# Kernel tuning notes

Measured on AMD Instinct MI355X. Metric: run time of the kernel, lower is better.

The kernel has to match this reference:

```python
import jax, jax.numpy as jnp
import numpy as np

N, C, HD, E, T, HS, WS = 8, 256, 8, 64, 16, 14, 14
S = HS * WS
EPS = 1e-5
FACTOR = 1.0 / np.sqrt(S * E).astype(np.float32)


def hswish(x):
    return x * jnp.clip(x + 3.0, 0.0, 6.0) * (1.0 / 6.0)


def _bn(x, g, b, m, v):
    shp = (1, -1, 1, 1, 1)
    scale = g / jnp.sqrt(v + EPS)
    return (x - m.reshape(shp)) * scale.reshape(shp) + b.reshape(shp)


def _dwconv(x, w):
    # depthwise Conv3d kernel (1,3,3), padding (0,1,1), groups=C
    return jax.lax.conv_general_dilated(
        x, w, window_strides=(1, 1, 1),
        padding=((0, 0), (1, 1), (1, 1)),
        dimension_numbers=('NCDHW', 'OIDHW', 'NCDHW'),
        feature_group_count=x.shape[1])


def _project(x, dw, g1, b1, m1, v1, pw, pb=None, bn2=None):
    h = hswish(_bn(_dwconv(x, dw), g1, b1, m1, v1))
    y = jnp.einsum('ncthw,oc->nothw', h, pw)
    if pb is not None:
        y = y + pb.reshape(1, -1, 1, 1, 1)
    if bn2 is not None:
        y = _bn(y, *bn2)
    return y


def setup_inputs() -> dict:
    key = jax.random.key(0)
    ks = jax.random.split(key, 8)
    d = {}
    d['x'] = jax.random.normal(ks[0], (N, C, T, HS, WS), jnp.float32)
    for name, k, out in (('theta', ks[1], HD * E), ('phi', ks[2], HD * E), ('g', ks[3], HD * C)):
        k1, k2 = jax.random.split(k)
        d[name + '_dw'] = jax.random.normal(k1, (C, 1, 1, 3, 3), jnp.float32) * 0.2
        d[name + '_bn1_g'] = jnp.ones((C,), jnp.float32)
        d[name + '_bn1_b'] = jnp.zeros((C,), jnp.float32)
        d[name + '_bn1_m'] = jnp.zeros((C,), jnp.float32)
        d[name + '_bn1_v'] = jnp.ones((C,), jnp.float32)
        d[name + '_pw'] = jax.random.normal(k2, (out, C), jnp.float32) * (1.0 / np.sqrt(C).astype(np.float32))
    d['theta_pb'] = jnp.zeros((HD * E,), jnp.float32)
    d['phi_pb'] = jnp.zeros((HD * E,), jnp.float32)
    d['g_bn2_g'] = jnp.ones((HD * C,), jnp.float32)
    d['g_bn2_b'] = jnp.zeros((HD * C,), jnp.float32)
    d['g_bn2_m'] = jnp.zeros((HD * C,), jnp.float32)
    d['g_bn2_v'] = jnp.ones((HD * C,), jnp.float32)
    d['heads_w'] = jax.random.normal(ks[4], (HD, HD), jnp.float32)
    return d


def reference(x, theta_dw, theta_bn1_g, theta_bn1_b, theta_bn1_m, theta_bn1_v, theta_pw, theta_pb,
              phi_dw, phi_bn1_g, phi_bn1_b, phi_bn1_m, phi_bn1_v, phi_pw, phi_pb,
              g_dw, g_bn1_g, g_bn1_b, g_bn1_m, g_bn1_v, g_pw,
              g_bn2_g, g_bn2_b, g_bn2_m, g_bn2_v, heads_w):
    th = _project(x, theta_dw, theta_bn1_g, theta_bn1_b, theta_bn1_m, theta_bn1_v, theta_pw, pb=theta_pb)
    ph = _project(x, phi_dw, phi_bn1_g, phi_bn1_b, phi_bn1_m, phi_bn1_v, phi_pw, pb=phi_pb)
    gg = hswish(_project(x, g_dw, g_bn1_g, g_bn1_b, g_bn1_m, g_bn1_v, g_pw,
                         bn2=(g_bn2_g, g_bn2_b, g_bn2_m, g_bn2_v)))
    TH = th.reshape(N, HD, E, T, S)   # theta features
    PH = ph.reshape(N, HD, E, T, S)   # phi features
    G5 = gg.reshape(N, HD, C, T, S)   # value features
    # adjacency over temporal nodes: [N,H,T,T]
    adj = jax.nn.softmax(FACTOR * jnp.einsum('nhets,nheus->nhtu', TH, PH), axis=-1)
    # GCN step: [N,H,T,C,S]
    gcn = hswish(jnp.einsum('nhtu,nhcus->nhtcs', adj, G5))
    # head-mix attention: [N,T,H]
    hf = gcn.mean(axis=(3, 4)).transpose(0, 2, 1)
    attn = jax.nn.softmax(hf @ heads_w, axis=-1)
    # combine heads: [N,C,T,S] -> [N,C,T,Hs,Ws]
    z = jnp.einsum('nhtcs,nth->ncts', gcn, attn).reshape(N, C, T, HS, WS)
    return hswish(x + z)
```

## Files before the change

### kernel.cpp

```cpp
#include <hip/hip_runtime.h>
#include <hip/hip_bf16.h>

typedef __hip_bfloat16 bf16;
typedef __attribute__((ext_vector_type(4))) float f32x4;
typedef __attribute__((ext_vector_type(8))) short s16x8;

#define DEV static __device__ __forceinline__

namespace {

constexpr float kEPS = 1e-5f;
constexpr float kFACTOR = 1.0f / 112.0f;

DEV float hswish_f(float v) { return v * fminf(fmaxf(v + 3.f, 0.f), 6.f) * (1.f / 6.f); }

__global__ void cvt_pw_kernel(const float* __restrict__ a,
                              const float* __restrict__ b,
                              const float* __restrict__ cG,
                              const float* __restrict__ g2g, const float* __restrict__ g2b,
                              const float* __restrict__ g2m, const float* __restrict__ g2v,
                              bf16* __restrict__ oa, bf16* __restrict__ ob,
                              bf16* __restrict__ oc, float* __restrict__ bnscl,
                              float* __restrict__ bnsft) {
  int i = blockIdx.x * 256 + threadIdx.x;
  if (i < 512 * 256) {
    oa[i] = __float2bfloat16(a[i]);
    ob[i] = __float2bfloat16(b[i]);
  }
  if (i < 2048 * 256) {
    int r = i >> 8, k = i & 255;
    int h = r >> 8, c = r & 255;
    oc[(c * 8 + h) * 256 + k] = __float2bfloat16(cG[i]);
  }
  if (i < 2048) {
    int c = i >> 3, h = i & 7, ref = h * 256 + c;
    float s = g2g[ref] * rsqrtf(g2v[ref] + kEPS);
    bnscl[i] = s;
    bnsft[i] = g2b[ref] - g2m[ref] * s;
  }
}

__global__ __launch_bounds__(256) void conv_kernel(
    const float* __restrict__ x,
    const float* __restrict__ tdw, const float* __restrict__ tg,
    const float* __restrict__ tb, const float* __restrict__ tm, const float* __restrict__ tv,
    const float* __restrict__ pdw, const float* __restrict__ pg,
    const float* __restrict__ pb, const float* __restrict__ pm, const float* __restrict__ pv,
    const float* __restrict__ gdw, const float* __restrict__ gG,
    const float* __restrict__ gb, const float* __restrict__ gm, const float* __restrict__ gv,
    bf16* __restrict__ h_t, bf16* __restrict__ h_p, bf16* __restrict__ h_g) {
  int bid = blockIdx.x;
  int cb = bid & 3, t = (bid >> 2) & 15, n = bid >> 6;
  int c0 = cb * 64;
  __shared__ float xs[64][197];
  __shared__ float wts[3][64][9];
  __shared__ float sc[3][64], sh[3][64];
  int tid = threadIdx.x;
  for (int i = tid; i < 64 * 9; i += 256) {
    int cl = i / 9, k = i % 9;
    wts[0][cl][k] = tdw[(c0 + cl) * 9 + k];
    wts[1][cl][k] = pdw[(c0 + cl) * 9 + k];
    wts[2][cl][k] = gdw[(c0 + cl) * 9 + k];
  }
  if (tid < 64) {
    int c = c0 + tid;
    float s0 = tg[c] * rsqrtf(tv[c] + kEPS);
    sc[0][tid] = s0; sh[0][tid] = tb[c] - tm[c] * s0;
    float s1 = pg[c] * rsqrtf(pv[c] + kEPS);
    sc[1][tid] = s1; sh[1][tid] = pb[c] - pm[c] * s1;
    float s2 = gG[c] * rsqrtf(gv[c] + kEPS);
    sc[2][tid] = s2; sh[2][tid] = gb[c] - gm[c] * s2;
  }
  const float* xb = x + ((size_t)(n * 256 + c0) * 16 + t) * 196;
  for (int i = tid; i < 64 * 196; i += 256) {
    int cl = i / 196, s = i % 196;
    xs[cl][s] = xb[(size_t)cl * 3136 + s];
  }
  __syncthreads();
  for (int i = tid; i < 64 * 196; i += 256) {
    int cl = i & 63, sp = i >> 6;
    int hs = sp / 14, wsp = sp % 14;
    float a0 = 0.f, a1 = 0.f, a2 = 0.f;
    #pragma unroll
    for (int dy = -1; dy <= 1; ++dy) {
      int yy = hs + dy;
      if (yy < 0 || yy >= 14) continue;
      #pragma unroll
      for (int dx = -1; dx <= 1; ++dx) {
        int xx = wsp + dx;
        if (xx < 0 || xx >= 14) continue;
        float v = xs[cl][yy * 14 + xx];
        int k = (dy + 1) * 3 + (dx + 1);
        a0 = fmaf(wts[0][cl][k], v, a0);
        a1 = fmaf(wts[1][cl][k], v, a1);
        a2 = fmaf(wts[2][cl][k], v, a2);
      }
    }
    a0 = hswish_f(a0 * sc[0][cl] + sh[0][cl]);
    a1 = hswish_f(a1 * sc[1][cl] + sh[1][cl]);
    a2 = hswish_f(a2 * sc[2][cl] + sh[2][cl]);
    size_t oidx = ((size_t)n * 3136 + t * 196 + sp) * 256 + c0 + cl;
    h_t[oidx] = __float2bfloat16(a0);
    h_p[oidx] = __float2bfloat16(a1);
    h_g[oidx] = __float2bfloat16(a2);
  }
}

__global__ __launch_bounds__(256) void gemm_op_kernel(
    const bf16* __restrict__ A,
    const bf16* __restrict__ B,
    bf16* __restrict__ D,
    const float* __restrict__ bias) {
  int mt = blockIdx.x, nt = blockIdx.y, n = blockIdx.z;
  __shared__ __align__(16) bf16 lds_a[128 * 64];
  __shared__ __align__(16) bf16 lds_b[64 * 64];
  int tid = threadIdx.x;
  int wid = tid >> 6, lane = tid & 63;
  int wr = wid >> 1, wc = wid & 1;
  int l15 = lane & 15, lh = lane >> 4;
  f32x4 acc[4][2];
  #pragma unroll
  for (int m = 0; m < 4; ++m)
    #pragma unroll
    for (int q = 0; q < 2; ++q) acc[m][q] = (f32x4){0.f, 0.f, 0.f, 0.f};
  const bf16* Ab = A + (size_t)mt * 128 * 256;
  const bf16* Bb = B + ((size_t)n * 3136 + (size_t)nt * 64) * 256;
  for (int k0 = 0; k0 < 256; k0 += 64) {
    #pragma unroll
    for (int it = 0; it < 4; ++it) {
      int g = tid + it * 256;
      int row = g >> 3, c16 = g & 7;
      int4 v = *(const int4*)(Ab + (size_t)row * 256 + k0 + c16 * 8);
      *(int4*)((char*)lds_a + row * 128 + ((c16 * 16) ^ ((row & 7) << 4))) = v;
    }
    #pragma unroll
    for (int it = 0; it < 2; ++it) {
      int g = tid + it * 256;
      int row = g >> 3, c16 = g & 7;
      int4 v = *(const int4*)(Bb + (size_t)row * 256 + k0 + c16 * 8);
      *(int4*)((char*)lds_b + row * 128 + ((c16 * 16) ^ ((row & 7) << 4))) = v;
    }
    __syncthreads();
    #pragma unroll
    for (int kk = 0; kk < 64; kk += 32) {
      s16x8 af[4], bfr[2];
      #pragma unroll
      for (int m = 0; m < 4; ++m) {
        int row = wr * 64 + m * 16 + l15;
        af[m] = *(const s16x8*)((const char*)lds_a + row * 128 +
                                (((kk + lh * 8) * 2) ^ ((row & 7) << 4)));
      }
      #pragma unroll
      for (int q = 0; q < 2; ++q) {
        int row = wc * 32 + q * 16 + l15;
        bfr[q] = *(const s16x8*)((const char*)lds_b + row * 128 +
                                 (((kk + lh * 8) * 2) ^ ((row & 7) << 4)));
      }
      #pragma unroll
      for (int m = 0; m < 4; ++m)
        #pragma unroll
        for (int q = 0; q < 2; ++q)
          acc[m][q] = __builtin_amdgcn_mfma_f32_16x16x32_bf16(af[m], bfr[q], acc[m][q], 0, 0, 0);
    }
    __syncthreads();
  }
  #pragma unroll
  for (int m = 0; m < 4; ++m) {
    #pragma unroll
    for (int q = 0; q < 2; ++q) {
      int col = wc * 32 + q * 16 + l15;
      #pragma unroll
      for (int r = 0; r < 4; ++r) {
        int row = wr * 64 + m * 16 + lh * 4 + r;
        float v = acc[m][q][r] + bias[mt * 128 + row];
        *(bf16*)((char*)lds_a + row * 128 + ((col * 2) ^ ((row & 7) << 4))) =
            __float2bfloat16(v);
      }
    }
  }
  __syncthreads();
  #pragma unroll
  for (int it = 0; it < 4; ++it) {
    int g = tid + it * 256;
    int row = g >> 3, cq = g & 7;
    int4 v = *(const int4*)((const char*)lds_a + row * 128 + ((cq * 16) ^ ((row & 7) << 4)));
    *(int4*)(D + ((size_t)n * 512 + mt * 128 + row) * 3136 + nt * 64 + cq * 8) = v;
  }
}

__global__ __launch_bounds__(256) void gemm_g_kernel(
    const bf16* __restrict__ A,
    const bf16* __restrict__ W,
    bf16* __restrict__ D,
    const float* __restrict__ bnscl, const float* __restrict__ bnsft) {
  int tsb = blockIdx.x, otb = blockIdx.y, n = blockIdx.z;
  __shared__ __align__(16) bf16 lds_a[64 * 64];
  __shared__ __align__(16) bf16 lds_b[128 * 64];
  int tid = threadIdx.x;
  int wid = tid >> 6, lane = tid & 63;
  int wr = wid >> 1, wc = wid & 1;
  int l15 = lane & 15, lh = lane >> 4;
  f32x4 acc[2][4];
  #pragma unroll
  for (int m = 0; m < 2; ++m)
    #pragma unroll
    for (int q = 0; q < 4; ++q) acc[m][q] = (f32x4){0.f, 0.f, 0.f, 0.f};
  const bf16* Ab = A + ((size_t)n * 3136 + (size_t)tsb * 64) * 256;
  const bf16* Wb = W + (size_t)otb * 128 * 256;
  for (int k0 = 0; k0 < 256; k0 += 64) {
    #pragma unroll
    for (int it = 0; it < 2; ++it) {
      int g = tid + it * 256;
      int row = g >> 3, c16 = g & 7;
      int4 v = *(const int4*)(Ab + (size_t)row * 256 + k0 + c16 * 8);
      *(int4*)((char*)lds_a + row * 128 + ((c16 * 16) ^ ((row & 7) << 4))) = v;
    }
    #pragma unroll
    for (int it = 0; it < 4; ++it) {
      int g = tid + it * 256;
      int row = g >> 3, c16 = g & 7;
      int4 v = *(const int4*)(Wb + (size_t)row * 256 + k0 + c16 * 8);
      *(int4*)((char*)lds_b + row * 128 + ((c16 * 16) ^ ((row & 7) << 4))) = v;
    }
    __syncthreads();
    #pragma unroll
    for (int kk = 0; kk < 64; kk += 32) {
      s16x8 af[2], bfr[4];
      #pragma unroll
      for (int m = 0; m < 2; ++m) {
        int row = wr * 32 + m * 16 + l15;
        af[m] = *(const s16x8*)((const char*)lds_a + row * 128 +
                                (((kk + lh * 8) * 2) ^ ((row & 7) << 4)));
      }
      #pragma unroll
      for (int q = 0; q < 4; ++q) {
        int row = wc * 64 + q * 16 + l15;
        bfr[q] = *(const s16x8*)((const char*)lds_b + row * 128 +
                                 (((kk + lh * 8) * 2) ^ ((row & 7) << 4)));
      }
      #pragma unroll
      for (int m = 0; m < 2; ++m)
        #pragma unroll
        for (int q = 0; q < 4; ++q)
          acc[m][q] = __builtin_amdgcn_mfma_f32_16x16x32_bf16(af[m], bfr[q], acc[m][q], 0, 0, 0);
    }
    __syncthreads();
  }
  #pragma unroll
  for (int q = 0; q < 4; ++q) {
    int ocol = wc * 64 + q * 16 + l15;
    float scl = bnscl[otb * 128 + ocol], sft = bnsft[otb * 128 + ocol];
    #pragma unroll
    for (int m = 0; m < 2; ++m) {
      #pragma unroll
      for (int r = 0; r < 4; ++r) {
        int row = wr * 32 + m * 16 + lh * 4 + r;
        float v = hswish_f(acc[m][q][r] * scl + sft);
        *(bf16*)((char*)lds_b + row * 256 + ((ocol * 2) ^ ((row & 7) << 4))) =
            __float2bfloat16(v);
      }
    }
  }
  __syncthreads();
  #pragma unroll
  for (int it = 0; it < 4; ++it) {
    int g = tid + it * 256;
    int row = g >> 4, cq = g & 15;
    int4 v = *(const int4*)((const char*)lds_b + row * 256 + ((cq * 16) ^ ((row & 7) << 4)));
    *(int4*)(D + ((size_t)n * 3136 + tsb * 64 + row) * 2048 + otb * 128 + cq * 8) = v;
  }
}

__global__ __launch_bounds__(256) void adj_accum_kernel(const bf16* __restrict__ th,
                                                        const bf16* __restrict__ ph,
                                                        float* __restrict__ adj_raw) {
  int bid = blockIdx.x;
  int eb = bid & 7, h = (bid >> 3) & 7, n = bid >> 6;
  __shared__ __align__(16) float As[16 * 196];
  __shared__ __align__(16) float Bs[16 * 196];
  int tid = threadIdx.x;
  int t = tid >> 4, u = tid & 15;
  float acc = 0.f;
  for (int e8 = 0; e8 < 8; ++e8) {
    int e = eb * 8 + e8;
    const bf16* tp = th + ((size_t)n * 512 + h * 64 + e) * 3136;
    const bf16* pp = ph + ((size_t)n * 512 + h * 64 + e) * 3136;
    __syncthreads();
    for (int i = tid; i < 3136; i += 256) {
      As[i] = __bfloat162float(tp[i]);
      Bs[i] = __bfloat162float(pp[i]);
    }
    __syncthreads();
    const float* ar = As + t * 196;
    const float* br = Bs + u * 196;
    #pragma unroll
    for (int j = 0; j < 49; ++j) {
      f32x4 a = *(const f32x4*)(ar + j * 4);
      f32x4 b = *(const f32x4*)(br + j * 4);
      acc = fmaf(a[0], b[0], acc); acc = fmaf(a[1], b[1], acc);
      acc = fmaf(a[2], b[2], acc); acc = fmaf(a[3], b[3], acc);
    }
  }
  atomicAdd(&adj_raw[((n * 8 + h) * 16 + t) * 16 + u], acc);
}

__global__ void adj_softmax_kernel(const float* __restrict__ raw, float* __restrict__ adj) {
  int r = blockIdx.x * 256 + threadIdx.x;
  if (r >= 1024) return;
  const float* p = raw + r * 16;
  float* q = adj + r * 16;
  float v[16], mx = -1e30f;
  #pragma unroll
  for (int u = 0; u < 16; ++u) { v[u] = p[u] * kFACTOR; mx = fmaxf(mx, v[u]); }
  float s = 0.f;
  #pragma unroll
  for (int u = 0; u < 16; ++u) { v[u] = __expf(v[u] - mx); s += v[u]; }
  float inv = 1.f / s;
  #pragma unroll
  for (int u = 0; u < 16; ++u) q[u] = v[u] * inv;
}

template <int EPI>
__global__ __launch_bounds__(256) void consume_kernel(
    const bf16* __restrict__ gg, const float* __restrict__ adj,
    const float* __restrict__ attn, float* __restrict__ hf,
    bf16* __restrict__ ztmp) {
  int s = blockIdx.x, oh = blockIdx.y, n = blockIdx.z;
  __shared__ __align__(16) bf16 ggL[16][1024];
  __shared__ __align__(16) float adjL[8][260];
  __shared__ __align__(16) char aux[4096];
  bf16(*zL)[128] = (bf16(*)[128])aux;
  float(*hfp)[8][16] = (float(*)[8][16])aux;
  int tid = threadIdx.x;
  int h = tid & 7;
  for (int i = tid; i < 2048; i += 256) adjL[i >> 8][i & 255] = adj[n * 2048 + i];
  const bf16* gsrc = gg + ((size_t)n * 3136 + s) * 2048 + oh * 1024;
  #pragma unroll
  for (int u = 0; u < 16; ++u)
    *(int2*)&ggL[u][tid * 4] = *(const int2*)(gsrc + (size_t)u * 196 * 2048 + tid * 4);
  float atn[16];
  if (EPI == 1) {
    #pragma unroll
    for (int t = 0; t < 16; ++t) atn[t] = attn[n * 128 + t * 8 + h];
  }
  __syncthreads();
  float hacc[16];
  if (EPI == 0) {
    #pragma unroll
    for (int t = 0; t < 16; ++t) hacc[t] = 0.f;
  }
  #pragma unroll
  for (int tb = 0; tb < 4; ++tb) {
    f32x4 aj[4][4];
    #pragma unroll
    for (int tt = 0; tt < 4; ++tt)
      #pragma unroll
      for (int u4 = 0; u4 < 4; ++u4)
        aj[tt][u4] = *(const f32x4*)&adjL[h][(tb * 4 + tt) * 16 + u4 * 4];
    #pragma unroll
    for (int k = 0; k < 4; ++k) {
      int op = tid + k * 256;
      float gv[16];
      #pragma unroll
      for (int u = 0; u < 16; ++u) gv[u] = __bfloat162float(ggL[u][op]);
      float zp[4];
      #pragma unroll
      for (int tt = 0; tt < 4; ++tt) {
        float z = 0.f;
        #pragma unroll
        for (int u4 = 0; u4 < 4; ++u4) {
          z = fmaf(aj[tt][u4][0], gv[u4 * 4 + 0], z);
          z = fmaf(aj[tt][u4][1], gv[u4 * 4 + 1], z);
          z = fmaf(aj[tt][u4][2], gv[u4 * 4 + 2], z);
          z = fmaf(aj[tt][u4][3], gv[u4 * 4 + 3], z);
        }
        if (EPI == 0) hacc[tb * 4 + tt] += hswish_f(z);
        else zp[tt] = atn[tb * 4 + tt] * hswish_f(z);
      }
      if (EPI == 1) {
        #pragma unroll
        for (int tt = 0; tt < 4; ++tt) {
          zp[tt] += __shfl_xor(zp[tt], 1);
          zp[tt] += __shfl_xor(zp[tt], 2);
          zp[tt] += __shfl_xor(zp[tt], 4);
        }
        if (h < 4)
          zL[tb * 4 + h][(tid >> 3) + k * 32] = __float2bfloat16(zp[h]);
      }
    }
  }
  if (EPI == 0) {
    #pragma unroll
    for (int t = 0; t < 16; ++t) {
      hacc[t] += __shfl_xor(hacc[t], 8);
      hacc[t] += __shfl_xor(hacc[t], 16);
      hacc[t] += __shfl_xor(hacc[t], 32);
    }
    if ((tid & 63) < 8) {
      #pragma unroll
      for (int t = 0; t < 16; ++t) hfp[tid >> 6][h][t] = hacc[t];
    }
    __syncthreads();
    if (tid < 128) {
      int h2 = tid & 7, t2 = tid >> 3;
      float v = hfp[0][h2][t2] + hfp[1][h2][t2] + hfp[2][h2][t2] + hfp[3][h2][t2];
      atomicAdd(&hf[n * 128 + t2 * 8 + h2], v);
    }
  } else {
    __syncthreads();
    int t = tid >> 4, cq = tid & 15;
    int4 v = *(const int4*)&zL[t][cq * 8];
    *(int4*)(ztmp + ((size_t)n * 3136 + t * 196 + s) * 256 + oh * 128 + cq * 8) = v;
  }
}

__global__ void attn_kernel(const float* __restrict__ hf, const float* __restrict__ hw,
                            float* __restrict__ attn) {
  int tid = threadIdx.x;
  if (tid >= 128) return;
  int n = tid >> 4, t = tid & 15;
  const float inv = 1.0f / (256.0f * 196.0f);
  float hm[8];
  #pragma unroll
  for (int h = 0; h < 8; ++h) hm[h] = hf[(n * 16 + t) * 8 + h] * inv;
  float o[8], mx = -1e30f;
  #pragma unroll
  for (int h2 = 0; h2 < 8; ++h2) {
    float s = 0.f;
    #pragma unroll
    for (int h = 0; h < 8; ++h) s = fmaf(hm[h], hw[h * 8 + h2], s);
    o[h2] = s; mx = fmaxf(mx, s);
  }
  float s = 0.f;
  #pragma unroll
  for (int h2 = 0; h2 < 8; ++h2) { o[h2] = __expf(o[h2] - mx); s += o[h2]; }
  float is = 1.f / s;
  #pragma unroll
  for (int h2 = 0; h2 < 8; ++h2) attn[(n * 16 + t) * 8 + h2] = o[h2] * is;
}

__global__ __launch_bounds__(256) void zres_kernel(const bf16* __restrict__ ztmp,
                                                   const float* __restrict__ x,
                                                   float* __restrict__ out) {
  int tsb = blockIdx.x, cb = blockIdx.y, n = blockIdx.z;
  __shared__ __align__(16) bf16 tile[64 * 64];
  int tid = threadIdx.x;
  #pragma unroll
  for (int it = 0; it < 2; ++it) {
    int g = tid + it * 256;
    int row = g >> 3, cq = g & 7;
    int4 v = *(const int4*)(ztmp + ((size_t)n * 3136 + tsb * 64 + row) * 256 + cb * 64 + cq * 8);
    *(int4*)((char*)tile + row * 128 + ((cq * 16) ^ ((row & 7) << 4))) = v;
  }
  __syncthreads();
  int cl = tid & 63, tq = tid >> 6;
  size_t obase = ((size_t)(n * 256 + cb * 64 + cl)) * 3136 + tsb * 64 + tq * 16;
  #pragma unroll
  for (int i = 0; i < 16; i += 4) {
    f32x4 xv = *(const f32x4*)(x + obase + i);
    f32x4 r;
    #pragma unroll
    for (int j = 0; j < 4; ++j) {
      int row = tq * 16 + i + j;
      unsigned short zb = *(const unsigned short*)((const char*)tile + row * 128 +
                                                   ((cl * 2) ^ ((row & 7) << 4)));
      float z = __uint_as_float((unsigned)zb << 16);
      r[j] = hswish_f(xv[j] + z);
    }
    *(f32x4*)(out + obase + i) = r;
  }
}

}

extern "C" void kernel_launch(void* const* d_in, const int* in_sizes, int n_in,
                              void* d_out, int out_size, void* d_ws, size_t ws_size,
                              hipStream_t stream) {
  const float* x       = (const float*)d_in[0];
  const float* t_dw    = (const float*)d_in[1];
  const float* t_g     = (const float*)d_in[2];
  const float* t_b     = (const float*)d_in[3];
  const float* t_m     = (const float*)d_in[4];
  const float* t_v     = (const float*)d_in[5];
  const float* t_pw    = (const float*)d_in[6];
  const float* p_dw    = (const float*)d_in[7];
  const float* p_g     = (const float*)d_in[8];
  const float* p_b     = (const float*)d_in[9];
  const float* p_m     = (const float*)d_in[10];
  const float* p_v     = (const float*)d_in[11];
  const float* p_pw    = (const float*)d_in[12];
  const float* g_dw    = (const float*)d_in[13];
  const float* g_g     = (const float*)d_in[14];
  const float* g_b     = (const float*)d_in[15];
  const float* g_m     = (const float*)d_in[16];
  const float* g_v     = (const float*)d_in[17];
  const float* g_pw    = (const float*)d_in[18];
  const float* t_pb    = (const float*)d_in[19];
  const float* p_pb    = (const float*)d_in[20];
  const float* g2_g    = (const float*)d_in[21];
  const float* g2_b    = (const float*)d_in[22];
  const float* g2_m    = (const float*)d_in[23];
  const float* g2_v    = (const float*)d_in[24];
  const float* heads_w = (const float*)d_in[25];
  float* out = (float*)d_out;
  (void)in_sizes; (void)n_in; (void)out_size; (void)ws_size;

  char* w = (char*)d_ws;
  size_t off = 0;
  auto take = [&](size_t bytes) {
    char* p = w + off;
    off = (off + bytes + 255) & ~(size_t)255;
    return p;
  };
  bf16* pwT = (bf16*)take(512 * 256 * 2);
  bf16* pwP = (bf16*)take(512 * 256 * 2);
  bf16* pwG = (bf16*)take(2048 * 256 * 2);
  float* bnscl = (float*)take(2048 * 4);
  float* bnsft = (float*)take(2048 * 4);
  bf16* hT  = (bf16*)take((size_t)8 * 3136 * 256 * 2);
  bf16* hP  = (bf16*)take((size_t)8 * 3136 * 256 * 2);
  bf16* hG  = (bf16*)take((size_t)8 * 3136 * 256 * 2);
  bf16* th  = (bf16*)take((size_t)8 * 512 * 3136 * 2);
  bf16* ph  = (bf16*)take((size_t)8 * 512 * 3136 * 2);
  bf16* gg  = (bf16*)take((size_t)8 * 3136 * 2048 * 2);
  float* adj_raw = (float*)take(1024 * 16 * 4);
  float* adj     = (float*)take(1024 * 16 * 4);
  float* hf      = (float*)take(1024 * 4);
  float* attn    = (float*)take(1024 * 4);
  bf16* ztmp = hT;

  hipMemsetAsync(adj_raw, 0, 1024 * 16 * 4, stream);
  hipMemsetAsync(hf, 0, 1024 * 4, stream);

  cvt_pw_kernel<<<2048, 256, 0, stream>>>(t_pw, p_pw, g_pw, g2_g, g2_b, g2_m, g2_v,
                                          pwT, pwP, pwG, bnscl, bnsft);
  conv_kernel<<<512, 256, 0, stream>>>(x, t_dw, t_g, t_b, t_m, t_v,
                                       p_dw, p_g, p_b, p_m, p_v,
                                       g_dw, g_g, g_b, g_m, g_v, hT, hP, hG);
  gemm_op_kernel<<<dim3(4, 49, 8), 256, 0, stream>>>(pwT, hT, th, t_pb);
  gemm_op_kernel<<<dim3(4, 49, 8), 256, 0, stream>>>(pwP, hP, ph, p_pb);
  gemm_g_kernel<<<dim3(49, 16, 8), 256, 0, stream>>>(hG, pwG, gg, bnscl, bnsft);
  adj_accum_kernel<<<512, 256, 0, stream>>>(th, ph, adj_raw);
  adj_softmax_kernel<<<4, 256, 0, stream>>>(adj_raw, adj);
  consume_kernel<0><<<dim3(196, 2, 8), 256, 0, stream>>>(gg, adj, nullptr, hf, nullptr);
  attn_kernel<<<1, 128, 0, stream>>>(hf, heads_w, attn);
  consume_kernel<1><<<dim3(196, 2, 8), 256, 0, stream>>>(gg, adj, attn, nullptr, ztmp);
  zres_kernel<<<dim3(49, 4, 8), 256, 0, stream>>>(ztmp, x, out);
}
```

Measured before the change: 452.5 us.

## Enlarge g-GEMM output tile, use direct global-to-LDS loads, remap block order

The g-projection GEMM now computes a 64x256 output tile per block instead of 64x128, with each wave covering all 64 rows and a 64-column slice, giving 16 accumulators per wave. Operand tiles are loaded with global_load_lds straight into LDS, with the swizzle applied on the global-address side, which skips the register round-trip. The grid is flattened to 1D with the batch index varying fastest so neighbouring blocks share weight tiles. The bigger tile raises register and LDS use, which may lower occupancy, and halves the block count.

```diff
diff --git a/kernel.cpp b/kernel.cpp
--- a/kernel.cpp
+++ b/kernel.cpp
@@ -13,6 +13,12 @@
 constexpr float kFACTOR = 1.0f / 112.0f;
 
 DEV float hswish_f(float v) { return v * fminf(fmaxf(v + 3.f, 0.f), 6.f) * (1.f / 6.f); }
+
+DEV void gload_lds16(const bf16* g, bf16* l) {
+  __builtin_amdgcn_global_load_lds(
+      (const __attribute__((address_space(1))) unsigned int*)g,
+      (__attribute__((address_space(3))) unsigned int*)l, 16, 0, 0);
+}
 
 __global__ void cvt_pw_kernel(const float* __restrict__ a,
                               const float* __restrict__ b,
@@ -193,53 +199,53 @@
     const bf16* __restrict__ W,
     bf16* __restrict__ D,
     const float* __restrict__ bnscl, const float* __restrict__ bnsft) {
-  int tsb = blockIdx.x, otb = blockIdx.y, n = blockIdx.z;
+  int bid = blockIdx.x;
+  int n = bid & 7, rem = bid >> 3;
+  int otb = rem / 49, tsb = rem % 49;
   __shared__ __align__(16) bf16 lds_a[64 * 64];
-  __shared__ __align__(16) bf16 lds_b[128 * 64];
+  __shared__ __align__(16) bf16 lds_b[256 * 64];
   int tid = threadIdx.x;
   int wid = tid >> 6, lane = tid & 63;
-  int wr = wid >> 1, wc = wid & 1;
   int l15 = lane & 15, lh = lane >> 4;
-  f32x4 acc[2][4];
-  #pragma unroll
-  for (int m = 0; m < 2; ++m)
+  f32x4 acc[4][4];
+  #pragma unroll
+  for (int m = 0; m < 4; ++m)
     #pragma unroll
     for (int q = 0; q < 4; ++q) acc[m][q] = (f32x4){0.f, 0.f, 0.f, 0.f};
   const bf16* Ab = A + ((size_t)n * 3136 + (size_t)tsb * 64) * 256;
-  const bf16* Wb = W + (size_t)otb * 128 * 256;
+  const bf16* Wb = W + (size_t)otb * 256 * 256;
+  int arow = tid >> 3, ac16 = tid & 7;
   for (int k0 = 0; k0 < 256; k0 += 64) {
     #pragma unroll
     for (int it = 0; it < 2; ++it) {
-      int g = tid + it * 256;
-      int row = g >> 3, c16 = g & 7;
-      int4 v = *(const int4*)(Ab + (size_t)row * 256 + k0 + c16 * 8);
-      *(int4*)((char*)lds_a + row * 128 + ((c16 * 16) ^ ((row & 7) << 4))) = v;
-    }
-    #pragma unroll
-    for (int it = 0; it < 4; ++it) {
-      int g = tid + it * 256;
-      int row = g >> 3, c16 = g & 7;
-      int4 v = *(const int4*)(Wb + (size_t)row * 256 + k0 + c16 * 8);
-      *(int4*)((char*)lds_b + row * 128 + ((c16 * 16) ^ ((row & 7) << 4))) = v;
+      int row = arow + it * 32;
+      gload_lds16(Ab + (size_t)row * 256 + k0 + ((ac16 ^ (row & 7)) * 8),
+                  lds_a + (size_t)(row * 8 + ac16) * 8);
+    }
+    #pragma unroll
+    for (int it = 0; it < 8; ++it) {
+      int row = arow + it * 32;
+      gload_lds16(Wb + (size_t)row * 256 + k0 + ((ac16 ^ (row & 7)) * 8),
+                  lds_b + (size_t)(row * 8 + ac16) * 8);
     }
     __syncthreads();
     #pragma unroll
     for (int kk = 0; kk < 64; kk += 32) {
-      s16x8 af[2], bfr[4];
-      #pragma unroll
-      for (int m = 0; m < 2; ++m) {
-        int row = wr * 32 + m * 16 + l15;
+      s16x8 af[4], bfr[4];
+      #pragma unroll
+      for (int m = 0; m < 4; ++m) {
+        int row = m * 16 + l15;
         af[m] = *(const s16x8*)((const char*)lds_a + row * 128 +
                                 (((kk + lh * 8) * 2) ^ ((row & 7) << 4)));
       }
       #pragma unroll
       for (int q = 0; q < 4; ++q) {
-        int row = wc * 64 + q * 16 + l15;
+        int row = wid * 64 + q * 16 + l15;
         bfr[q] = *(const s16x8*)((const char*)lds_b + row * 128 +
                                  (((kk + lh * 8) * 2) ^ ((row & 7) << 4)));
       }
       #pragma unroll
-      for (int m = 0; m < 2; ++m)
+      for (int m = 0; m < 4; ++m)
         #pragma unroll
         for (int q = 0; q < 4; ++q)
           acc[m][q] = __builtin_amdgcn_mfma_f32_16x16x32_bf16(af[m], bfr[q], acc[m][q], 0, 0, 0);
@@ -248,26 +254,26 @@
   }
   #pragma unroll
   for (int q = 0; q < 4; ++q) {
-    int ocol = wc * 64 + q * 16 + l15;
-    float scl = bnscl[otb * 128 + ocol], sft = bnsft[otb * 128 + ocol];
-    #pragma unroll
-    for (int m = 0; m < 2; ++m) {
+    int ocol = wid * 64 + q * 16 + l15;
+    float scl = bnscl[otb * 256 + ocol], sft = bnsft[otb * 256 + ocol];
+    #pragma unroll
+    for (int m = 0; m < 4; ++m) {
       #pragma unroll
       for (int r = 0; r < 4; ++r) {
-        int row = wr * 32 + m * 16 + lh * 4 + r;
+        int row = m * 16 + lh * 4 + r;
         float v = hswish_f(acc[m][q][r] * scl + sft);
-        *(bf16*)((char*)lds_b + row * 256 + ((ocol * 2) ^ ((row & 7) << 4))) =
+        *(bf16*)((char*)lds_b + row * 512 + ((ocol * 2) ^ ((row & 7) << 4))) =
             __float2bfloat16(v);
       }
     }
   }
   __syncthreads();
   #pragma unroll
-  for (int it = 0; it < 4; ++it) {
+  for (int it = 0; it < 8; ++it) {
     int g = tid + it * 256;
-    int row = g >> 4, cq = g & 15;
-    int4 v = *(const int4*)((const char*)lds_b + row * 256 + ((cq * 16) ^ ((row & 7) << 4)));
-    *(int4*)(D + ((size_t)n * 3136 + tsb * 64 + row) * 2048 + otb * 128 + cq * 8) = v;
+    int row = g >> 5, cq = g & 31;
+    int4 v = *(const int4*)((const char*)lds_b + row * 512 + ((cq * 16) ^ ((row & 7) << 4)));
+    *(int4*)(D + ((size_t)n * 3136 + tsb * 64 + row) * 2048 + otb * 256 + cq * 8) = v;
   }
 }
 
@@ -539,7 +545,7 @@
                                        g_dw, g_g, g_b, g_m, g_v, hT, hP, hG);
   gemm_op_kernel<<<dim3(4, 49, 8), 256, 0, stream>>>(pwT, hT, th, t_pb);
   gemm_op_kernel<<<dim3(4, 49, 8), 256, 0, stream>>>(pwP, hP, ph, p_pb);
-  gemm_g_kernel<<<dim3(49, 16, 8), 256, 0, stream>>>(hG, pwG, gg, bnscl, bnsft);
+  gemm_g_kernel<<<3136, 256, 0, stream>>>(hG, pwG, gg, bnscl, bnsft);
   adj_accum_kernel<<<512, 256, 0, stream>>>(th, ph, adj_raw);
   adj_softmax_kernel<<<4, 256, 0, stream>>>(adj_raw, adj);
   consume_kernel<0><<<dim3(196, 2, 8), 256, 0, stream>>>(gg, adj, nullptr, hf, nullptr);
```

Result: faster. 443.0 us (-2.1%).
